# Optimization experiments

Measured on AMD Instinct MI355X. Metric: run time of the kernel, lower is better.

The kernel has to match this reference:

```python
import jax, jax.numpy as jnp
import numpy as np

NUM_HEADS = 8
EPS = 1e-12  # torch F.normalize default eps


def _l2norm(t):
    # t / max(||t||_2, eps) along last axis (matches F.normalize)
    n = jnp.sqrt(jnp.sum(t * t, axis=-1, keepdims=True))
    return t / jnp.maximum(n, EPS)


def setup_inputs() -> dict:
    key = jax.random.key(0)
    k1, k2, k3 = jax.random.split(key, 3)
    B, N, C = 8, 1024, 768
    x = jax.random.normal(k1, (B, N, C), dtype=jnp.float32)
    w_qkv = jax.random.normal(k2, (C, 3 * C), dtype=jnp.float32) * 0.02
    temperature = jnp.ones((NUM_HEADS, 1, 1), dtype=jnp.float32)
    w_proj = jax.random.normal(k3, (C, C), dtype=jnp.float32) * 0.02
    b_proj = jnp.zeros((C,), dtype=jnp.float32)
    return {"x": x, "w_qkv": w_qkv, "temperature": temperature,
            "w_proj": w_proj, "b_proj": b_proj}


def reference(x, w_qkv, temperature, w_proj, b_proj):
    B, N, C = x.shape
    H = NUM_HEADS
    hd = C // H
    # qkv projection (no bias), split into q,k,v of shape [B,H,N,hd]
    qkv = (x @ w_qkv).reshape(B, N, 3, H, hd)
    qkv = jnp.transpose(qkv, (2, 0, 3, 1, 4))  # [3,B,H,N,hd]
    q, k, v = qkv[0], qkv[1], qkv[2]
    q = _l2norm(q)
    k = _l2norm(k)
    # NOTE: code (unlike canonical XCA) does NOT transpose q/k, so attn is [B,H,N,N]
    attn = jnp.einsum('bhnd,bhmd->bhnm', q, k) * temperature  # temp broadcasts over B
    attn = jax.nn.softmax(attn, axis=-1)
    out = jnp.einsum('bhnm,bhmd->bhnd', attn, v)  # [B,H,N,hd]
    out = jnp.transpose(out, (0, 2, 1, 3)).reshape(B, N, C)
    return out @ w_proj + b_proj
```

## Files before the change

kernel.cpp:

```cpp
#include <hip/hip_runtime.h>
#include <math.h>

typedef __attribute__((ext_vector_type(8))) short bf16x8;
typedef __attribute__((ext_vector_type(4))) float f32x4;
typedef __attribute__((ext_vector_type(4))) unsigned int u32x4;
typedef unsigned short u16;
typedef unsigned int u32;


__device__ __forceinline__ u16 f2b(float f) {
  u32 u = __float_as_uint(f);
  return (u16)((u + 0x7fffu + ((u >> 16) & 1u)) >> 16);
}
__device__ __forceinline__ float b2f(u16 h) {
  return __uint_as_float(((u32)h) << 16);
}
__device__ __forceinline__ int swz(int m) { return (m ^ (m >> 2)) & 3; }

__device__ __forceinline__ void async16(const void* g, void* l) {
  __builtin_amdgcn_global_load_lds((const __attribute__((address_space(1))) u32*)g,
                                   (__attribute__((address_space(3))) u32*)l, 16, 0, 0);
}

__global__ __launch_bounds__(256) void prep_kernel(const float* __restrict__ x,
                                                   const float* __restrict__ w_qkv,
                                                   const float* __restrict__ w_proj,
                                                   u16* __restrict__ xb,
                                                   u16* __restrict__ wqkvT,
                                                   u16* __restrict__ wprojT) {
  __shared__ float t[32][33];
  const int blk = blockIdx.x;
  if (blk < 6144) {
    const int idx = blk * 256 + threadIdx.x;
    const float4 v = ((const float4*)x)[idx];
    uint2 o;
    o.x = (u32)f2b(v.x) | ((u32)f2b(v.y) << 16);
    o.y = (u32)f2b(v.z) | ((u32)f2b(v.w) << 16);
    ((uint2*)xb)[idx] = o;
    return;
  }
  const float* in; u16* out; int R, C, bx, by;
  if (blk < 6144 + 1728) {
    const int rem = blk - 6144;
    in = w_qkv; out = wqkvT; R = 768; C = 2304; bx = rem % 72; by = rem / 72;
  } else {
    const int rem = blk - 6144 - 1728;
    in = w_proj; out = wprojT; R = 768; C = 768; bx = rem % 24; by = rem / 24;
  }
  const int c0 = bx * 32, r0 = by * 32;
  const int tc = threadIdx.x & 31, tr = threadIdx.x >> 5;
#pragma unroll
  for (int j = 0; j < 4; ++j)
    t[tr + j * 8][tc] = in[(size_t)(r0 + tr + j * 8) * C + c0 + tc];
  __syncthreads();
#pragma unroll
  for (int j = 0; j < 4; ++j)
    out[(size_t)(c0 + tr + j * 8) * R + r0 + tc] = f2b(t[tc][tr + j * 8]);
}

template<int NT>
__device__ __forceinline__ void gemm_core(const u16* __restrict__ A,
                                          const u16* __restrict__ Bt,
                                          int m0, int n0, f32x4 acc[4][NT / 32]) {
  constexpr int JT = NT / 32;
  constexpr int NINST = (512 + NT * 4) / 256;
  __shared__ u16 Sm[(512 + NT * 4) * 8];
  const int tid = threadIdx.x;
  const int w = tid >> 6, lane = tid & 63;
  const int i15 = lane & 15, quad = lane >> 4;
  const int wm = (w >> 1) * 64, wn = (w & 1) * (NT / 2);
  const int sw = quad ^ swz(i15);

#pragma unroll
  for (int i = 0; i < 4; ++i)
#pragma unroll
    for (int j = 0; j < JT; ++j) acc[i][j] = (f32x4){0.f, 0.f, 0.f, 0.f};

  for (int k0 = 0; k0 < 768; k0 += 32) {
    __syncthreads();
#pragma unroll
    for (int inst = 0; inst < NINST; ++inst) {
      const int s = inst * 256 + tid;
      const u16* src;
      if (inst < 2) {
        const int m = s >> 2, e = s & 3;
        src = A + ((size_t)(m0 + m) * 768 + k0 + (e ^ swz(m)) * 8);
      } else {
        const int s2 = s - 512;
        const int n = s2 >> 2, e = s2 & 3;
        src = Bt + ((size_t)(n0 + n) * 768 + k0 + (e ^ swz(n)) * 8);
      }
      async16(src, (void*)(Sm + (size_t)(inst * 256 + w * 64) * 8));
    }
    __syncthreads();
    bf16x8 af[4], bf[JT];
#pragma unroll
    for (int i = 0; i < 4; ++i)
      af[i] = *(const bf16x8*)(Sm + ((size_t)(wm + i * 16 + i15) * 4 + sw) * 8);
#pragma unroll
    for (int j = 0; j < JT; ++j)
      bf[j] = *(const bf16x8*)(Sm + ((size_t)512 + (wn + j * 16 + i15) * 4 + sw) * 8);
#pragma unroll
    for (int i = 0; i < 4; ++i)
#pragma unroll
      for (int j = 0; j < JT; ++j)
        acc[i][j] = __builtin_amdgcn_mfma_f32_16x16x32_bf16(af[i], bf[j], acc[i][j], 0, 0, 0);
  }
}

__global__ __launch_bounds__(256, 3) void qkv_gemm_kernel(
    const u16* __restrict__ xb, const u16* __restrict__ wT,
    const float* __restrict__ temp,
    u16* __restrict__ q, u16* __restrict__ k, u16* __restrict__ vT) {
  f32x4 acc[4][6];
  const int bid = blockIdx.x;
  const int xcd = bid & 7, slot = bid >> 3;
  const int mb = xcd * 8 + slot / 12, nb = slot % 12;
  const int m0 = mb * 128, n0 = nb * 192;
  gemm_core<192>(xb, wT, m0, n0, acc);

  const int tid = threadIdx.x, w = tid >> 6, lane = tid & 63;
  const int i15 = lane & 15, quad = lane >> 4;
  const int wm = (w >> 1) * 64;
  const int three = nb >> 2;
  const int h = ((nb & 3) << 1) + (w & 1);

  if (three < 2) {
    u16* dst = three ? k : q;
    const float sc_extra = three ? 1.f : temp[h];
#pragma unroll
    for (int it = 0; it < 4; ++it) {
#pragma unroll
      for (int r = 0; r < 4; ++r) {
        float s = 0.f;
#pragma unroll
        for (int jt = 0; jt < 6; ++jt) s += acc[it][jt][r] * acc[it][jt][r];
        s += __shfl_xor(s, 1); s += __shfl_xor(s, 2);
        s += __shfl_xor(s, 4); s += __shfl_xor(s, 8);
        const float scale = sc_extra / fmaxf(sqrtf(s), 1e-12f);
        const int m = m0 + wm + it * 16 + quad * 4 + r;
        const int b = m >> 10, n = m & 1023;
        u16* rowp = dst + ((size_t)(b * 8 + h) * 1024 + n) * 96;
#pragma unroll
        for (int jt = 0; jt < 6; ++jt)
          rowp[jt * 16 + i15] = f2b(acc[it][jt][r] * scale);
      }
    }
  } else {
#pragma unroll
    for (int it = 0; it < 4; ++it) {
      const int mb4 = m0 + wm + it * 16 + quad * 4;
      const int b = mb4 >> 10, nbase = mb4 & 1023;
#pragma unroll
      for (int jt = 0; jt < 6; ++jt) {
        const int d = jt * 16 + i15;
        uint2 pk;
        pk.x = (u32)f2b(acc[it][jt][0]) | ((u32)f2b(acc[it][jt][1]) << 16);
        pk.y = (u32)f2b(acc[it][jt][2]) | ((u32)f2b(acc[it][jt][3]) << 16);
        *(uint2*)(vT + ((size_t)(b * 8 + h) * 96 + d) * 1024 + nbase) = pk;
      }
    }
  }
}

__global__ __launch_bounds__(512, 4) void attn_kernel(
    const u16* __restrict__ q, const u16* __restrict__ kk,
    const u16* __restrict__ vT, u16* __restrict__ ctx) {
  __shared__ u16 smem[32768];
  const int tid = threadIdx.x, w = tid >> 6, lane = tid & 63;
  const int i15 = lane & 15, quad = lane >> 4;
  const int xs = swz(i15);
  const int bh = blockIdx.x & 63, qbase = (blockIdx.x >> 6) * 128;
  const int b = bh >> 3, h = bh & 7;
  u16* Pw = smem + 24576 + w * 1024;

  bf16x8 qf[3];
  {
    const int qrow = qbase + w * 16 + i15;
    const u16* qp = q + ((size_t)bh * 1024 + qrow) * 96 + quad * 8;
#pragma unroll
    for (int c = 0; c < 3; ++c) qf[c] = *(const bf16x8*)(qp + c * 32);
  }

  const u16* gsrc[3]; int gstep[3];
#pragma unroll
  for (int inst = 0; inst < 3; ++inst) {
    const int s = inst * 512 + tid;
    if (s < 768) {
      const int key6 = (s & 255) >> 2, c = s >> 8;
      const int e = c * 4 + ((s & 3) ^ swz(key6));
      gsrc[inst] = kk + ((size_t)bh * 1024 + key6) * 96 + e * 8;
      gstep[inst] = 64 * 96;
    } else {
      const int s2 = s - 768, r = s2 >> 2;
      const int c2 = (r >= 96), d = r - 96 * c2;
      gsrc[inst] = vT + ((size_t)bh * 96 + d) * 1024 + c2 * 32 + ((s2 & 3) ^ swz(d)) * 8;
      gstep[inst] = 64;
    }
  }

#pragma unroll
  for (int inst = 0; inst < 3; ++inst)
    async16(gsrc[inst], (void*)(smem + (size_t)(inst * 512 + w * 64) * 8));

  f32x4 o[6];
#pragma unroll
  for (int dt = 0; dt < 6; ++dt) o[dt] = (f32x4){0.f, 0.f, 0.f, 0.f};
  float l = 0.f;

  for (int t = 0; t < 16; ++t) {
    __syncthreads();
    const u16* KVs = smem + (t & 1) * 12288;
    if (t < 15) {
      u16* dst = smem + ((t + 1) & 1) * 12288;
#pragma unroll
      for (int inst = 0; inst < 3; ++inst) {
        gsrc[inst] += gstep[inst];
        async16(gsrc[inst], (void*)(dst + (size_t)(inst * 512 + w * 64) * 8));
      }
    }
#pragma unroll
    for (int kt = 0; kt < 4; ++kt) {
      bf16x8 af[3];
#pragma unroll
      for (int c = 0; c < 3; ++c)
        af[c] = *(const bf16x8*)(KVs + ((size_t)((c * 64 + kt * 16 + i15) * 4) + (quad ^ xs)) * 8);
      f32x4 s = (f32x4){0.f, 0.f, 0.f, 0.f};
#pragma unroll
      for (int c = 0; c < 3; ++c)
        s = __builtin_amdgcn_mfma_f32_16x16x32_bf16(af[c], qf[c], s, 0, 0, 0);
      const float e0 = __expf(s[0]), e1 = __expf(s[1]);
      const float e2 = __expf(s[2]), e3 = __expf(s[3]);
      l += (e0 + e1) + (e2 + e3);
      uint2 pk;
      pk.x = (u32)f2b(e0) | ((u32)f2b(e1) << 16);
      pk.y = (u32)f2b(e2) | ((u32)f2b(e3) << 16);
      const int pg = (kt & 1) * 2 + (quad >> 1);
      *(uint2*)(Pw + (size_t)(((kt >> 1) * 16 + i15) * 4 + (pg ^ xs)) * 8
                    + (quad & 1) * 4) = pk;
    }
#pragma unroll
    for (int c2 = 0; c2 < 2; ++c2) {
      const bf16x8 pa = *(const bf16x8*)(Pw + (size_t)((c2 * 16 + i15) * 4 + (quad ^ xs)) * 8);
#pragma unroll
      for (int dt = 0; dt < 6; ++dt) {
        const bf16x8 vb = *(const bf16x8*)(KVs +
            ((size_t)(768 + (c2 * 96 + dt * 16 + i15) * 4) + (quad ^ xs)) * 8);
        o[dt] = __builtin_amdgcn_mfma_f32_16x16x32_bf16(pa, vb, o[dt], 0, 0, 0);
      }
    }
  }

  l += __shfl_xor(l, 16); l += __shfl_xor(l, 32);
  __syncthreads();
  u16* scr = smem + w * 1664;
#pragma unroll
  for (int r = 0; r < 4; ++r) {
    const float linv = 1.f / __shfl(l, quad * 4 + r);
    const int row16 = quad * 4 + r;
#pragma unroll
    for (int dt = 0; dt < 6; ++dt)
      scr[row16 * 104 + dt * 16 + i15] = f2b(o[dt][r] * linv);
  }
#pragma unroll
  for (int jj = 0; jj < 3; ++jj) {
    const int id = jj * 64 + lane;
    const int row16 = id / 12, g = id - row16 * 12;
    const int grow = b * 1024 + qbase + w * 16 + row16;
    *(uint4*)(ctx + (size_t)grow * 768 + h * 96 + g * 8) =
        *(const uint4*)(scr + row16 * 104 + g * 8);
  }
}

__global__ __launch_bounds__(256, 4) void proj_gemm_kernel(
    const u16* __restrict__ ctx, const u16* __restrict__ wT,
    const float* __restrict__ bias, float* __restrict__ out) {
  f32x4 acc[4][2];
  const int bid = blockIdx.x;
  const int xcd = bid & 7, slot = bid >> 3;
  const int mb = xcd * 8 + slot / 12, nb = slot % 12;
  const int m0 = mb * 128, n0 = nb * 64;
  gemm_core<64>(ctx, wT, m0, n0, acc);

  const int tid = threadIdx.x, w = tid >> 6, lane = tid & 63;
  const int i15 = lane & 15, quad = lane >> 4;
  const int wm = (w >> 1) * 64, wn = (w & 1) * 32;
#pragma unroll
  for (int jt = 0; jt < 2; ++jt) {
    const int c = n0 + wn + jt * 16 + i15;
    const float bb = bias[c];
#pragma unroll
    for (int it = 0; it < 4; ++it) {
#pragma unroll
      for (int r = 0; r < 4; ++r) {
        const int m = m0 + wm + it * 16 + quad * 4 + r;
        out[(size_t)m * 768 + c] = acc[it][jt][r] + bb;
      }
    }
  }
}

extern "C" void kernel_launch(void* const* d_in, const int* in_sizes, int n_in,
                              void* d_out, int out_size, void* d_ws, size_t ws_size,
                              hipStream_t stream) {
  const float* x      = (const float*)d_in[0];
  const float* w_qkv  = (const float*)d_in[1];
  const float* temp   = (const float*)d_in[2];
  const float* w_proj = (const float*)d_in[3];
  const float* b_proj = (const float*)d_in[4];

  u16* ws      = (u16*)d_ws;
  u16* xb      = ws;
  u16* wqkvT   = xb + 6291456;
  u16* qb      = wqkvT + 1769472;
  u16* kb      = qb + 6291456;
  u16* vTb     = kb + 6291456;
  u16* ctxb    = vTb + 6291456;
  u16* wprojT  = ctxb + 6291456;

  prep_kernel<<<8448, 256, 0, stream>>>(x, w_qkv, w_proj, xb, wqkvT, wprojT);
  qkv_gemm_kernel<<<768, 256, 0, stream>>>(xb, wqkvT, temp, qb, kb, vTb);
  attn_kernel<<<512, 512, 0, stream>>>(qb, kb, vTb, ctxb);
  proj_gemm_kernel<<<768, 256, 0, stream>>>(ctxb, wprojT, b_proj, (float*)d_out);
}
```

Measured before the change: 181.0 us.

## Double-buffer LDS tiles in GEMM core to overlap global loads with MFMA

The shared GEMM core now keeps two LDS stages. It issues the async global-to-LDS loads for the next K-slice before running the MFMAs on the current slice, which cuts one barrier per iteration. Source pointers are computed once and advanced by the K step each iteration, so per-iteration address math goes away. The cost is twice the LDS per block, which may limit occupancy alongside the launch bounds. The design also relies on the barrier waiting for outstanding async loads before each stage is read.

```diff
diff --git a/kernel.cpp b/kernel.cpp
--- a/kernel.cpp
+++ b/kernel.cpp
@@ -63,8 +63,9 @@
                                           const u16* __restrict__ Bt,
                                           int m0, int n0, f32x4 acc[4][NT / 32]) {
   constexpr int JT = NT / 32;
-  constexpr int NINST = (512 + NT * 4) / 256;
-  __shared__ u16 Sm[(512 + NT * 4) * 8];
+  constexpr int NG = 512 + NT * 4;
+  constexpr int NINST = NG / 256;
+  __shared__ u16 Sm[2 * NG * 8];
   const int tid = threadIdx.x;
   const int w = tid >> 6, lane = tid & 63;
   const int i15 = lane & 15, quad = lane >> 4;
@@ -76,30 +77,42 @@
 #pragma unroll
     for (int j = 0; j < JT; ++j) acc[i][j] = (f32x4){0.f, 0.f, 0.f, 0.f};
 
-  for (int k0 = 0; k0 < 768; k0 += 32) {
+  const u16* gsrc[NINST];
+#pragma unroll
+  for (int inst = 0; inst < NINST; ++inst) {
+    const int s = inst * 256 + tid;
+    if (s < 512) {
+      const int m = s >> 2, e = s & 3;
+      gsrc[inst] = A + ((size_t)(m0 + m) * 768 + (e ^ swz(m)) * 8);
+    } else {
+      const int s2 = s - 512;
+      const int n = s2 >> 2, e = s2 & 3;
+      gsrc[inst] = Bt + ((size_t)(n0 + n) * 768 + (e ^ swz(n)) * 8);
+    }
+  }
+
+#pragma unroll
+  for (int inst = 0; inst < NINST; ++inst)
+    async16(gsrc[inst], (void*)(Sm + (size_t)(inst * 256 + w * 64) * 8));
+
+  for (int t = 0; t < 24; ++t) {
     __syncthreads();
-#pragma unroll
-    for (int inst = 0; inst < NINST; ++inst) {
-      const int s = inst * 256 + tid;
-      const u16* src;
-      if (inst < 2) {
-        const int m = s >> 2, e = s & 3;
-        src = A + ((size_t)(m0 + m) * 768 + k0 + (e ^ swz(m)) * 8);
-      } else {
-        const int s2 = s - 512;
-        const int n = s2 >> 2, e = s2 & 3;
-        src = Bt + ((size_t)(n0 + n) * 768 + k0 + (e ^ swz(n)) * 8);
-      }
-      async16(src, (void*)(Sm + (size_t)(inst * 256 + w * 64) * 8));
-    }
-    __syncthreads();
+    const u16* buf = Sm + (size_t)(t & 1) * NG * 8;
+    if (t < 23) {
+      u16* dst = Sm + (size_t)((t + 1) & 1) * NG * 8;
+#pragma unroll
+      for (int inst = 0; inst < NINST; ++inst) {
+        gsrc[inst] += 32;
+        async16(gsrc[inst], (void*)(dst + (size_t)(inst * 256 + w * 64) * 8));
+      }
+    }
     bf16x8 af[4], bf[JT];
 #pragma unroll
     for (int i = 0; i < 4; ++i)
-      af[i] = *(const bf16x8*)(Sm + ((size_t)(wm + i * 16 + i15) * 4 + sw) * 8);
+      af[i] = *(const bf16x8*)(buf + ((size_t)(wm + i * 16 + i15) * 4 + sw) * 8);
 #pragma unroll
     for (int j = 0; j < JT; ++j)
-      bf[j] = *(const bf16x8*)(Sm + ((size_t)512 + (wn + j * 16 + i15) * 4 + sw) * 8);
+      bf[j] = *(const bf16x8*)(buf + ((size_t)512 + (wn + j * 16 + i15) * 4 + sw) * 8);
 #pragma unroll
     for (int i = 0; i < 4; ++i)
 #pragma unroll
```

New measurement: 183.0 us. About the same (+1.1%).
